# Kernel tuning notes

Hardware: AMD Instinct MI355X
Metric: run time of the kernel (lower is better)

The kernel has to match this reference:

```python
import jax, jax.numpy as jnp
import numpy as np

B, N, K = 4, 2048, 32
H, DS, DE = 128, 128, 128
NUM_IN = DS + DE + H  # 384
SCALE = 30.0
EPS = 1e-5


def setup_inputs() -> dict:
    key = jax.random.key(0)
    ks = jax.random.split(key, 9)
    s = 0.05
    return {
        "h_S": jax.random.normal(ks[0], (B, N, DS), jnp.float32),
        "h_V": jax.random.normal(ks[1], (B, N, H), jnp.float32),
        "h_E": jax.random.normal(ks[2], (B, N, K, DE), jnp.float32),
        "E_idx": jax.random.randint(ks[3], (B, N, K), 0, N, jnp.int64),
        "mask_attend": jnp.ones((B, N, K), jnp.float32),
        "W1_w": jax.random.normal(ks[4], (H + NUM_IN, H), jnp.float32) * s,
        "W1_b": jnp.zeros((H,), jnp.float32),
        "W2_w": jax.random.normal(ks[5], (H, H), jnp.float32) * s,
        "W2_b": jnp.zeros((H,), jnp.float32),
        "ln_g": jnp.ones((H,), jnp.float32),
        "ln_b": jnp.zeros((H,), jnp.float32),
    }


def gather_nodes(nodes, idx):
    # nodes: [B, N, D], idx: [B, N, K] -> [B, N, K, D]
    b, n, k = idx.shape
    d = nodes.shape[-1]
    flat = jnp.broadcast_to(idx.reshape(b, n * k, 1), (b, n * k, d))
    return jnp.take_along_axis(nodes, flat, axis=1).reshape(b, n, k, d)


def layer_norm(x, g, b):
    mu = jnp.mean(x, axis=-1, keepdims=True)
    var = jnp.var(x, axis=-1, keepdims=True)
    return (x - mu) * jax.lax.rsqrt(var + EPS) * g + b


def reference(h_S, h_V, h_E, E_idx, mask_attend, W1_w, W1_b, W2_w, W2_b, ln_g, ln_b):
    # h_ES = cat(h_E, gather(h_S))  -> [B,N,K,DE+DS]
    h_ES = jnp.concatenate([h_E, gather_nodes(h_S, E_idx)], axis=-1)
    # h_EXV = cat(h_ES, gather(h_V)) -> [B,N,K,DE+DS+H], masked
    h_EXV = jnp.concatenate([h_ES, gather_nodes(h_V, E_idx)], axis=-1)
    h_EXV = mask_attend[..., None] * h_EXV
    # h_EV = cat(h_V expanded, h_EXV) -> [B,N,K,H+NUM_IN]
    h_V_exp = jnp.broadcast_to(h_V[:, :, None, :], (h_V.shape[0], h_V.shape[1], K, h_V.shape[2]))
    h_EV = jnp.concatenate([h_V_exp, h_EXV], axis=-1)
    # per-edge 2-layer MLP (exact GELU as torch.nn.GELU)
    h = jax.nn.gelu(jnp.einsum("bnkf,fh->bnkh", h_EV, W1_w) + W1_b, approximate=False)
    h_message = jnp.einsum("bnkh,hg->bnkg", h, W2_w) + W2_b
    dh = jnp.sum(h_message, axis=-2) / SCALE
    # dropout is identity in eval mode
    return layer_norm(h_V + dh, ln_g, ln_b)
```

## Files before the change

### kernel.cpp

```cpp
#include <hip/hip_runtime.h>
#include <math.h>

typedef float f32x4 __attribute__((ext_vector_type(4)));
typedef short s16x8 __attribute__((ext_vector_type(8)));
typedef unsigned u32x4 __attribute__((ext_vector_type(4)));

#define N_NODES 2048
#define KEDGE 32
#define HDIM 128
#define SB() __builtin_amdgcn_sched_barrier(0)

__device__ __forceinline__ short f2bf(float f){
  unsigned u = __builtin_bit_cast(unsigned, f);
  u += 0x7fffu + ((u >> 16) & 1u);
  return (short)(u >> 16);
}
__device__ __forceinline__ float bf2f(short s){
  unsigned u = ((unsigned)(unsigned short)s) << 16;
  return __builtin_bit_cast(float, u);
}
__device__ __forceinline__ unsigned cvt_pk_bf16(float a, float b){
  unsigned r;
  asm("v_cvt_pk_bf16_f32 %0, %1, %2" : "=v"(r) : "v"(a), "v"(b));
  return r;
}
__device__ __forceinline__ float fast_gelu(float x){
  float t = x * (-2.3022078f - 0.1029527f * x * x);
  float e = __builtin_amdgcn_exp2f(t);
  return x * __builtin_amdgcn_rcpf(1.0f + e);
}
__device__ __forceinline__ void gld16(const void* g, void* l){
  __builtin_amdgcn_global_load_lds(
      (const __attribute__((address_space(1))) void*)g,
      (__attribute__((address_space(3))) void*)l, 16, 0, 0);
}
__device__ __forceinline__ f32x4 mfma16(s16x8 a, s16x8 b, f32x4 c){
  return __builtin_amdgcn_mfma_f32_16x16x32_bf16(a, b, c, 0, 0, 0);
}

__global__ void prep1(const float* __restrict__ W1, const float* __restrict__ W2,
                      short* __restrict__ W1f, short* __restrict__ W2f,
                      unsigned* __restrict__ flag){
  if (blockIdx.x == 320){
    if (threadIdx.x == 0) *flag = 0u;
    return;
  }
  int t = blockIdx.x * 256 + threadIdx.x;
  if (t < 65536){
    int ks = t >> 12, r = t & 4095;
    int ct = r >> 9;  r &= 511;
    int lane = r >> 3, j = r & 7;
    int k = ks*32 + (lane>>4)*8 + j;
    int n = ct*16 + (lane&15);
    W1f[t] = f2bf(W1[k*128 + n]);
  } else if (t < 81920){
    int t2 = t - 65536;
    int ks = t2 >> 12, r = t2 & 4095;
    int ct = r >> 9;  r &= 511;
    int lane = r >> 3, j = r & 7;
    int k = ks*32 + (lane>>4)*8 + j;
    int n = ct*16 + (lane&15);
    W2f[t2] = f2bf(W2[k*128 + n]);
  }
}

__global__ __launch_bounds__(256)
void prep2(const float* __restrict__ hS, const float* __restrict__ hV,
           const float* __restrict__ b1, const short* __restrict__ W1f,
           short* __restrict__ Zb, unsigned* __restrict__ UHb,
           const unsigned* __restrict__ Ei_u, unsigned* __restrict__ flag){
  if (blockIdx.x >= 128){
    int t = ((int)blockIdx.x - 128)*256 + threadIdx.x;
    unsigned v = Ei_u[2*t + 1];
    unsigned long long m = __ballot(v != 0u);
    if ((threadIdx.x & 63) == 0 && m) atomicOr(flag, 1u);
    return;
  }
  const int tid = threadIdx.x;
  const int w = tid >> 6, lane = tid & 63, l15 = lane & 15, lg = lane >> 4;
  const int nb = ((int)blockIdx.x*4 + w)*16;

  f32x4 accz[8], accu[8];
  #pragma unroll
  for (int ct = 0; ct < 8; ++ct){ accz[ct] = (f32x4){0,0,0,0}; accu[ct] = (f32x4){0,0,0,0}; }

  #pragma unroll
  for (int ks = 0; ks < 4; ++ks){
    const float* p = hS + (long)(nb + l15)*128 + ks*32 + lg*8;
    float4 x = *(const float4*)p, y = *(const float4*)(p + 4);
    u32x4 pk;
    pk[0] = cvt_pk_bf16(x.x, x.y); pk[1] = cvt_pk_bf16(x.z, x.w);
    pk[2] = cvt_pk_bf16(y.x, y.y); pk[3] = cvt_pk_bf16(y.z, y.w);
    s16x8 a = __builtin_bit_cast(s16x8, pk);
    #pragma unroll
    for (int ct = 0; ct < 8; ++ct){
      s16x8 bf = *(const s16x8*)(W1f + (8+ks)*4096 + ct*512 + lane*8);
      accz[ct] = mfma16(a, bf, accz[ct]);
    }
  }
  #pragma unroll
  for (int ks = 0; ks < 4; ++ks){
    const float* p = hV + (long)(nb + l15)*128 + ks*32 + lg*8;
    float4 x = *(const float4*)p, y = *(const float4*)(p + 4);
    u32x4 pk;
    pk[0] = cvt_pk_bf16(x.x, x.y); pk[1] = cvt_pk_bf16(x.z, x.w);
    pk[2] = cvt_pk_bf16(y.x, y.y); pk[3] = cvt_pk_bf16(y.z, y.w);
    s16x8 a = __builtin_bit_cast(s16x8, pk);
    #pragma unroll
    for (int ct = 0; ct < 8; ++ct){
      s16x8 bfd = *(const s16x8*)(W1f + (12+ks)*4096 + ct*512 + lane*8);
      accz[ct] = mfma16(a, bfd, accz[ct]);
      s16x8 bfa = *(const s16x8*)(W1f + (0+ks)*4096 + ct*512 + lane*8);
      accu[ct] = mfma16(a, bfa, accu[ct]);
    }
  }

  float b1v[8];
  #pragma unroll
  for (int ct = 0; ct < 8; ++ct) b1v[ct] = b1[ct*16 + l15];

  #pragma unroll
  for (int ct = 0; ct < 8; ++ct)
    #pragma unroll
    for (int i = 0; i < 4; ++i){
      const long row = nb + lg*4 + i;
      Zb[row*128 + ct*16 + l15] = f2bf(accz[ct][i]);
      unsigned u16 = (unsigned)(unsigned short)f2bf(accu[ct][i] + b1v[ct]);
      unsigned h16 = (unsigned)(unsigned short)f2bf(hV[row*128 + ct*16 + l15]);
      UHb[row*128 + l15*8 + ct] = u16 | (h16 << 16);
    }
}

__global__ __launch_bounds__(256, 1)
void fusedF(const float* __restrict__ hE, const int* __restrict__ Eidx,
            const float* __restrict__ mask, const short* __restrict__ W1f,
            const short* __restrict__ W2f, const short* __restrict__ Zb,
            const unsigned* __restrict__ UHb, const unsigned* __restrict__ idx_flag,
            const float* __restrict__ W2b, const float* __restrict__ lng,
            const float* __restrict__ lnb, float* __restrict__ out)
{
  __shared__ __align__(16) char smem[69632];

  const int tid  = threadIdx.x;
  const int w    = tid >> 6;
  const int lane = tid & 63;
  const int l15  = lane & 15;
  const int lg   = lane >> 4;

  const int bid  = (int)blockIdx.x;
  const int bswz = (bid & 7)*64 + (bid >> 3);
  const int n0 = (bswz * 4 + w) * 4;
  const long zrow0 = (long)(n0 >> 11) * N_NODES;
  char* mybuf  = smem + w*16384;
  short* vpark = (short*)(smem + 65536 + w*1024);

  const int rr = lane >> 5;
  const unsigned t0 = (unsigned)((rr << 9) | (((lane & 31) << 4) ^ (rr << 4)));

  s16x8 wf[4][8];
  #pragma unroll
  for (int ks = 0; ks < 4; ++ks)
    #pragma unroll
    for (int ct = 0; ct < 8; ++ct)
      wf[ks][ct] = *(const s16x8*)(W1f + (4+ks)*4096 + ct*512 + lane*8);
  SB();

  s16x8 ifr[2];
  #pragma unroll
  for (int c2 = 0; c2 < 2; ++c2){
    const int active = ((lg >> 1) == c2);
    const int j = l15 - 8*(lg & 1);
    s16x8 f;
    #pragma unroll
    for (int e = 0; e < 8; ++e)
      f[e] = (active && j == e) ? (short)0x3F80 : (short)0;
    ifr[c2] = f;
  }

  const int is64 = (*idx_flag == 0u) ? 1 : 0;

  int e0, eZ;
  {
    const int ea = n0*32 + l15;
    const int eb = n0*32 + 16 + l15;
    e0 = Eidx[ea << is64];
    eZ = Eidx[eb << is64];
  }
  float maskC = mask[n0*32 + l15];
  s16x8 uhC[2];
  uhC[0] = *(const s16x8*)((const short*)UHb + (long)n0*256 + l15*16);
  uhC[1] = *(const s16x8*)((const short*)UHb + (long)n0*256 + l15*16 + 8);
  SB();
  #pragma unroll
  for (int q = 0; q < 8; ++q){
    const unsigned off = (unsigned)(q*1024) | (t0 ^ (unsigned)((2*q & 6) << 4));
    gld16((const char*)hE + (size_t)n0*16384 + off, mybuf + q*1024);
  }
  SB();
  s16x8 zbC[4];
  #pragma unroll
  for (int ks = 0; ks < 4; ++ks)
    zbC[ks] = *(const s16x8*)(Zb + (zrow0 + e0)*128 + ks*32 + lg*8);
  SB();
  asm volatile("s_waitcnt vmcnt(0)" ::: "memory");
  SB();

  float vacc[8];
  #pragma unroll
  for (int ct = 0; ct < 8; ++ct) vacc[ct] = 0.f;

  #pragma unroll
  for (int t = 0; t < 8; ++t){
    const int tn = t + 1;
    float maskN = 0.f; s16x8 uhN0{}, uhN1{}; int eN = 0;
    s16x8 zbN0{}, zbN1{}, zbN2{}, zbN3{};
    if (t < 7){
      const int nn_n = n0 + (tn >> 1);
      SB();
      maskN = mask[nn_n*32 + (tn&1)*16 + l15];
      uhN0 = *(const s16x8*)((const short*)UHb + (long)nn_n*256 + l15*16);
      uhN1 = *(const s16x8*)((const short*)UHb + (long)nn_n*256 + l15*16 + 8);
      {
        const int t2 = t + 2;
        const int nz = (t2 <= 7) ? (n0 + (t2>>1)) : n0;
        const int hz = (t2 <= 7) ? (t2&1) : 0;
        eN = Eidx[(nz*32 + hz*16 + l15) << is64];
      }
      SB();
      {
        const size_t eb = (size_t)nn_n*16384 + (size_t)(tn&1)*8192;
        char* sbuf = mybuf + (tn&1)*8192;
        #pragma unroll
        for (int q = 0; q < 8; ++q){
          const unsigned off = (unsigned)(q*1024) | (t0 ^ (unsigned)((2*q & 6) << 4));
          gld16((const char*)hE + eb + off, sbuf + q*1024);
        }
      }
      SB();
      zbN0 = *(const s16x8*)(Zb + (zrow0 + eZ)*128 + 0*32 + lg*8);
      zbN1 = *(const s16x8*)(Zb + (zrow0 + eZ)*128 + 1*32 + lg*8);
      zbN2 = *(const s16x8*)(Zb + (zrow0 + eZ)*128 + 2*32 + lg*8);
      zbN3 = *(const s16x8*)(Zb + (zrow0 + eZ)*128 + 3*32 + lg*8);
      SB();
      asm volatile("s_waitcnt vmcnt(20)" ::: "memory");
      SB();
    } else {
      asm volatile("s_waitcnt vmcnt(0)" ::: "memory");
      SB();
    }

    __builtin_amdgcn_s_setprio(1);

    f32x4 acc1[8];
    #pragma unroll
    for (int ct = 0; ct < 8; ++ct) acc1[ct] = (f32x4){0,0,0,0};

    s16x8 afr[4];
    const char* cbuf = mybuf + (t&1)*8192;
    const int sw = (l15 & 7) << 4;
    const int rowb = l15 * 512;
    #pragma unroll
    for (int ks = 0; ks < 4; ++ks){
      const int c0 = ks*128 + lg*32;
      float4 ex = *(const float4*)(cbuf + rowb + (c0 ^ sw));
      float4 ey = *(const float4*)(cbuf + rowb + ((c0 + 16) ^ sw));
      u32x4 pk;
      pk[0] = cvt_pk_bf16(ex.x, ex.y); pk[1] = cvt_pk_bf16(ex.z, ex.w);
      pk[2] = cvt_pk_bf16(ey.x, ey.y); pk[3] = cvt_pk_bf16(ey.z, ey.w);
      afr[ks] = __builtin_bit_cast(s16x8, pk);
      #pragma unroll
      for (int ct = 0; ct < 8; ++ct)
        acc1[ct] = mfma16(afr[ks], wf[ks][ct], acc1[ct]);
    }

    if (t < 7){
      asm volatile("s_waitcnt vmcnt(16)" ::: "memory");
      SB();
    }

    #pragma unroll
    for (int ks = 0; ks < 4; ++ks)
      #pragma unroll
      for (int c2 = 0; c2 < 2; ++c2)
        acc1[ks*2 + c2] = mfma16(zbC[ks], ifr[c2], acc1[ks*2 + c2]);

    float uv[8];
    #pragma unroll
    for (int ct = 0; ct < 4; ++ct){ uv[ct] = bf2f(uhC[0][2*ct]); uv[4+ct] = bf2f(uhC[1][2*ct]); }
    float mi[4];
    #pragma unroll
    for (int i = 0; i < 4; ++i) mi[i] = __shfl(maskC, lg*4 + i, 64);
    #pragma unroll
    for (int ct = 0; ct < 8; ++ct)
      #pragma unroll
      for (int i = 0; i < 4; ++i)
        vacc[ct] += fast_gelu(uv[ct] + mi[i]*acc1[ct][i]);

    __builtin_amdgcn_s_setprio(0);

    if (t & 1){
      short* vl = vpark + (t >> 1)*128;
      #pragma unroll
      for (int ct = 0; ct < 8; ++ct){
        float s = vacc[ct];
        s += __shfl_xor(s, 16, 64);
        s += __shfl_xor(s, 32, 64);
        vacc[ct] = 0.f;
        if (ct == lg*2 || ct == lg*2 + 1)
          vl[ct*16 + l15] = f2bf(s);
      }
    }

    if (t < 7){
      maskC = maskN; uhC[0] = uhN0; uhC[1] = uhN1; eZ = eN;
      zbC[0] = zbN0; zbC[1] = zbN1; zbC[2] = zbN2; zbC[3] = zbN3;
    }
  }

  asm volatile("s_waitcnt lgkmcnt(0)" ::: "memory");
  SB();

  float w2b8[8], lngv[2], lnbv[2];
  #pragma unroll
  for (int ct = 0; ct < 8; ++ct) w2b8[ct] = W2b[ct*16 + l15];
  #pragma unroll
  for (int q = 0; q < 2; ++q){
    const int c = (lg*2 + q)*16 + l15;
    lngv[q] = lng[c]; lnbv[q] = lnb[c];
  }

  #pragma unroll
  for (int nd = 0; nd < 4; ++nd){
    const short* vl = vpark + nd*128;
    f32x4 acc2[8];
    #pragma unroll
    for (int ct = 0; ct < 8; ++ct) acc2[ct] = (f32x4){0,0,0,0};
    #pragma unroll
    for (int ks2 = 0; ks2 < 4; ++ks2){
      s16x8 av = *(const s16x8*)(vl + ks2*32 + lg*8);
      const short* wb2 = W2f + ks2*4096 + lane*8;
      #pragma unroll
      for (int ct = 0; ct < 8; ++ct){
        s16x8 bf = *(const s16x8*)(wb2 + ct*512);
        acc2[ct] = mfma16(av, bf, acc2[ct]);
      }
    }

    s16x8 uh0 = *(const s16x8*)((const short*)UHb + (long)(n0+nd)*256 + l15*16);
    s16x8 uh1 = *(const s16x8*)((const short*)UHb + (long)(n0+nd)*256 + l15*16 + 8);
    float hv[8];
    #pragma unroll
    for (int ct = 0; ct < 4; ++ct){ hv[ct] = bf2f(uh0[2*ct+1]); hv[4+ct] = bf2f(uh1[2*ct+1]); }

    float res[8], vs = 0.f, vq = 0.f;
    #pragma unroll
    for (int ct = 0; ct < 8; ++ct){
      float dh  = (acc2[ct][0] + 32.0f * w2b8[ct]) * (1.0f/30.0f);
      float val = hv[ct] + dh;
      res[ct] = val;
      vs += val; vq += val*val;
    }
    vs += __shfl_xor(vs, 1, 64);  vs += __shfl_xor(vs, 2, 64);
    vs += __shfl_xor(vs, 4, 64);  vs += __shfl_xor(vs, 8, 64);
    vq += __shfl_xor(vq, 1, 64);  vq += __shfl_xor(vq, 2, 64);
    vq += __shfl_xor(vq, 4, 64);  vq += __shfl_xor(vq, 8, 64);
    const float mu  = vs * (1.0f/128.0f);
    const float var = vq * (1.0f/128.0f) - mu*mu;
    const float rs  = rsqrtf(var + 1e-5f);

    const long nodeoff = (long)(n0 + nd) * HDIM;
    #pragma unroll
    for (int q = 0; q < 2; ++q){
      const int ct = lg*2 + q;
      out[nodeoff + ct*16 + l15] = (res[ct] - mu) * rs * lngv[q] + lnbv[q];
    }
  }
}

extern "C" void kernel_launch(void* const* d_in, const int* in_sizes, int n_in,
                              void* d_out, int out_size, void* d_ws, size_t ws_size,
                              hipStream_t stream) {
  const float* hS  = (const float*)d_in[0];
  const float* hV  = (const float*)d_in[1];
  const float* hE  = (const float*)d_in[2];
  const int*   Ei  = (const int*)d_in[3];
  const float* mk  = (const float*)d_in[4];
  const float* W1w = (const float*)d_in[5];
  const float* W1b = (const float*)d_in[6];
  const float* W2w = (const float*)d_in[7];
  const float* W2b = (const float*)d_in[8];
  const float* lng = (const float*)d_in[9];
  const float* lnb = (const float*)d_in[10];

  short* W1f = (short*)d_ws;
  short* W2f = W1f + 65536;
  unsigned* flag = (unsigned*)((char*)d_ws + 163840);
  short* Zb = (short*)((char*)d_ws + 164096);
  unsigned* UHb = (unsigned*)((char*)d_ws + 2261248);

  prep1<<<321, 256, 0, stream>>>(W1w, W2w, W1f, W2f, flag);
  prep2<<<640, 256, 0, stream>>>(hS, hV, W1b, W1f, Zb, UHb, (const unsigned*)Ei, flag);
  fusedF<<<512, 256, 0, stream>>>(hE, Ei, mk, W1f, W2f, Zb, UHb, flag,
                                  W2b, lng, lnb, (float*)d_out);
}
```

Before: 88.30 us.

## Split each node group across wave pairs, halving per-wave columns and doubling grid

Each group of four nodes is now handled by a pair of waves. Each wave computes half of the output columns, loads half of the hE tile into a shared LDS buffer, and holds half of the W1 fragments in registers. Block barriers synchronize the two halves on the shared LDS buffers, and the grid doubles to 1024 blocks. The aim is lower register and LDS pressure per wave and more parallelism and occupancy, at the cost of extra block-wide barriers and redundant per-team index and mask loads.

```diff
diff --git a/kernel.cpp b/kernel.cpp
--- a/kernel.cpp
+++ b/kernel.cpp
@@ -139,30 +139,33 @@
             const float* __restrict__ W2b, const float* __restrict__ lng,
             const float* __restrict__ lnb, float* __restrict__ out)
 {
-  __shared__ __align__(16) char smem[69632];
+  __shared__ __align__(16) char smem[34816];
 
   const int tid  = threadIdx.x;
   const int w    = tid >> 6;
+  const int team = w >> 1;
+  const int half = w & 1;
+  const int ctb  = half * 4;
   const int lane = tid & 63;
   const int l15  = lane & 15;
   const int lg   = lane >> 4;
 
   const int bid  = (int)blockIdx.x;
-  const int bswz = (bid & 7)*64 + (bid >> 3);
-  const int n0 = (bswz * 4 + w) * 4;
+  const int bswz = (bid & 7)*128 + (bid >> 3);
+  const int n0 = (bswz*2 + team) * 4;
   const long zrow0 = (long)(n0 >> 11) * N_NODES;
-  char* mybuf  = smem + w*16384;
-  short* vpark = (short*)(smem + 65536 + w*1024);
+  char* mybuf  = smem + team*16384;
+  short* vpark = (short*)(smem + 32768 + team*1024);
 
   const int rr = lane >> 5;
   const unsigned t0 = (unsigned)((rr << 9) | (((lane & 31) << 4) ^ (rr << 4)));
 
-  s16x8 wf[4][8];
+  s16x8 wf[4][4];
   #pragma unroll
   for (int ks = 0; ks < 4; ++ks)
     #pragma unroll
-    for (int ct = 0; ct < 8; ++ct)
-      wf[ks][ct] = *(const s16x8*)(W1f + (4+ks)*4096 + ct*512 + lane*8);
+    for (int c = 0; c < 4; ++c)
+      wf[ks][c] = *(const s16x8*)(W1f + (4+ks)*4096 + (ctb+c)*512 + lane*8);
   SB();
 
   s16x8 ifr[2];
@@ -187,39 +190,38 @@
     eZ = Eidx[eb << is64];
   }
   float maskC = mask[n0*32 + l15];
-  s16x8 uhC[2];
-  uhC[0] = *(const s16x8*)((const short*)UHb + (long)n0*256 + l15*16);
-  uhC[1] = *(const s16x8*)((const short*)UHb + (long)n0*256 + l15*16 + 8);
-  SB();
-  #pragma unroll
-  for (int q = 0; q < 8; ++q){
-    const unsigned off = (unsigned)(q*1024) | (t0 ^ (unsigned)((2*q & 6) << 4));
-    gld16((const char*)hE + (size_t)n0*16384 + off, mybuf + q*1024);
-  }
-  SB();
-  s16x8 zbC[4];
-  #pragma unroll
-  for (int ks = 0; ks < 4; ++ks)
-    zbC[ks] = *(const s16x8*)(Zb + (zrow0 + e0)*128 + ks*32 + lg*8);
+  s16x8 uhC = *(const s16x8*)((const short*)UHb + (long)n0*256 + l15*16 + ctb*2);
+  SB();
+  #pragma unroll
+  for (int j = 0; j < 4; ++j){
+    const int qq = half*4 + j;
+    const unsigned off = (unsigned)(qq*1024) | (t0 ^ (unsigned)((2*qq & 6) << 4));
+    gld16((const char*)hE + (size_t)n0*16384 + off, mybuf + qq*1024);
+  }
+  SB();
+  s16x8 zbC[2];
+  #pragma unroll
+  for (int kk = 0; kk < 2; ++kk)
+    zbC[kk] = *(const s16x8*)(Zb + (zrow0 + e0)*128 + (half*2+kk)*32 + lg*8);
   SB();
   asm volatile("s_waitcnt vmcnt(0)" ::: "memory");
   SB();
-
-  float vacc[8];
-  #pragma unroll
-  for (int ct = 0; ct < 8; ++ct) vacc[ct] = 0.f;
+  __builtin_amdgcn_s_barrier();
+
+  float vacc[4];
+  #pragma unroll
+  for (int c = 0; c < 4; ++c) vacc[c] = 0.f;
 
   #pragma unroll
   for (int t = 0; t < 8; ++t){
     const int tn = t + 1;
-    float maskN = 0.f; s16x8 uhN0{}, uhN1{}; int eN = 0;
-    s16x8 zbN0{}, zbN1{}, zbN2{}, zbN3{};
+    float maskN = 0.f; s16x8 uhN{}; int eN = 0;
+    s16x8 zbN0{}, zbN1{};
     if (t < 7){
       const int nn_n = n0 + (tn >> 1);
       SB();
       maskN = mask[nn_n*32 + (tn&1)*16 + l15];
-      uhN0 = *(const s16x8*)((const short*)UHb + (long)nn_n*256 + l15*16);
-      uhN1 = *(const s16x8*)((const short*)UHb + (long)nn_n*256 + l15*16 + 8);
+      uhN = *(const s16x8*)((const short*)UHb + (long)nn_n*256 + l15*16 + ctb*2);
       {
         const int t2 = t + 2;
         const int nz = (t2 <= 7) ? (n0 + (t2>>1)) : n0;
@@ -231,31 +233,30 @@
         const size_t eb = (size_t)nn_n*16384 + (size_t)(tn&1)*8192;
         char* sbuf = mybuf + (tn&1)*8192;
         #pragma unroll
-        for (int q = 0; q < 8; ++q){
-          const unsigned off = (unsigned)(q*1024) | (t0 ^ (unsigned)((2*q & 6) << 4));
-          gld16((const char*)hE + eb + off, sbuf + q*1024);
+        for (int j = 0; j < 4; ++j){
+          const int qq = half*4 + j;
+          const unsigned off = (unsigned)(qq*1024) | (t0 ^ (unsigned)((2*qq & 6) << 4));
+          gld16((const char*)hE + eb + off, sbuf + qq*1024);
         }
       }
       SB();
-      zbN0 = *(const s16x8*)(Zb + (zrow0 + eZ)*128 + 0*32 + lg*8);
-      zbN1 = *(const s16x8*)(Zb + (zrow0 + eZ)*128 + 1*32 + lg*8);
-      zbN2 = *(const s16x8*)(Zb + (zrow0 + eZ)*128 + 2*32 + lg*8);
-      zbN3 = *(const s16x8*)(Zb + (zrow0 + eZ)*128 + 3*32 + lg*8);
-      SB();
-      asm volatile("s_waitcnt vmcnt(20)" ::: "memory");
+      zbN0 = *(const s16x8*)(Zb + (zrow0 + eZ)*128 + (half*2+0)*32 + lg*8);
+      zbN1 = *(const s16x8*)(Zb + (zrow0 + eZ)*128 + (half*2+1)*32 + lg*8);
+      SB();
+      asm volatile("s_waitcnt vmcnt(11)" ::: "memory");
       SB();
     } else {
       asm volatile("s_waitcnt vmcnt(0)" ::: "memory");
       SB();
     }
+    __builtin_amdgcn_s_barrier();
 
     __builtin_amdgcn_s_setprio(1);
 
-    f32x4 acc1[8];
-    #pragma unroll
-    for (int ct = 0; ct < 8; ++ct) acc1[ct] = (f32x4){0,0,0,0};
-
-    s16x8 afr[4];
+    f32x4 acc1[4];
+    #pragma unroll
+    for (int c = 0; c < 4; ++c) acc1[c] = (f32x4){0,0,0,0};
+
     const char* cbuf = mybuf + (t&1)*8192;
     const int sw = (l15 & 7) << 4;
     const int rowb = l15 * 512;
@@ -267,58 +268,59 @@
       u32x4 pk;
       pk[0] = cvt_pk_bf16(ex.x, ex.y); pk[1] = cvt_pk_bf16(ex.z, ex.w);
       pk[2] = cvt_pk_bf16(ey.x, ey.y); pk[3] = cvt_pk_bf16(ey.z, ey.w);
-      afr[ks] = __builtin_bit_cast(s16x8, pk);
+      s16x8 a = __builtin_bit_cast(s16x8, pk);
       #pragma unroll
-      for (int ct = 0; ct < 8; ++ct)
-        acc1[ct] = mfma16(afr[ks], wf[ks][ct], acc1[ct]);
+      for (int c = 0; c < 4; ++c)
+        acc1[c] = mfma16(a, wf[ks][c], acc1[c]);
     }
 
     if (t < 7){
-      asm volatile("s_waitcnt vmcnt(16)" ::: "memory");
-      SB();
-    }
-
-    #pragma unroll
-    for (int ks = 0; ks < 4; ++ks)
+      asm volatile("s_waitcnt vmcnt(9)" ::: "memory");
+      SB();
+    }
+
+    #pragma unroll
+    for (int kk = 0; kk < 2; ++kk)
       #pragma unroll
       for (int c2 = 0; c2 < 2; ++c2)
-        acc1[ks*2 + c2] = mfma16(zbC[ks], ifr[c2], acc1[ks*2 + c2]);
-
-    float uv[8];
-    #pragma unroll
-    for (int ct = 0; ct < 4; ++ct){ uv[ct] = bf2f(uhC[0][2*ct]); uv[4+ct] = bf2f(uhC[1][2*ct]); }
+        acc1[kk*2 + c2] = mfma16(zbC[kk], ifr[c2], acc1[kk*2 + c2]);
+
+    float uv[4];
+    #pragma unroll
+    for (int c = 0; c < 4; ++c) uv[c] = bf2f(uhC[2*c]);
     float mi[4];
     #pragma unroll
     for (int i = 0; i < 4; ++i) mi[i] = __shfl(maskC, lg*4 + i, 64);
     #pragma unroll
-    for (int ct = 0; ct < 8; ++ct)
+    for (int c = 0; c < 4; ++c)
       #pragma unroll
       for (int i = 0; i < 4; ++i)
-        vacc[ct] += fast_gelu(uv[ct] + mi[i]*acc1[ct][i]);
+        vacc[c] += fast_gelu(uv[c] + mi[i]*acc1[c][i]);
 
     __builtin_amdgcn_s_setprio(0);
 
     if (t & 1){
       short* vl = vpark + (t >> 1)*128;
       #pragma unroll
-      for (int ct = 0; ct < 8; ++ct){
-        float s = vacc[ct];
+      for (int c = 0; c < 4; ++c){
+        float s = vacc[c];
         s += __shfl_xor(s, 16, 64);
         s += __shfl_xor(s, 32, 64);
-        vacc[ct] = 0.f;
-        if (ct == lg*2 || ct == lg*2 + 1)
-          vl[ct*16 + l15] = f2bf(s);
+        vacc[c] = 0.f;
+        if (lg == c)
+          vl[(ctb + c)*16 + l15] = f2bf(s);
       }
     }
 
     if (t < 7){
-      maskC = maskN; uhC[0] = uhN0; uhC[1] = uhN1; eZ = eN;
-      zbC[0] = zbN0; zbC[1] = zbN1; zbC[2] = zbN2; zbC[3] = zbN3;
+      maskC = maskN; uhC = uhN; eZ = eN;
+      zbC[0] = zbN0; zbC[1] = zbN1;
     }
   }
 
   asm volatile("s_waitcnt lgkmcnt(0)" ::: "memory");
   SB();
+  __builtin_amdgcn_s_barrier();
 
   float w2b8[8], lngv[2], lnbv[2];
   #pragma unroll
@@ -330,7 +332,8 @@
   }
 
   #pragma unroll
-  for (int nd = 0; nd < 4; ++nd){
+  for (int j = 0; j < 2; ++j){
+    const int nd = half*2 + j;
     const short* vl = vpark + nd*128;
     f32x4 acc2[8];
     #pragma unroll
@@ -350,7 +353,7 @@
     s16x8 uh1 = *(const s16x8*)((const short*)UHb + (long)(n0+nd)*256 + l15*16 + 8);
     float hv[8];
     #pragma unroll
-    for (int ct = 0; ct < 4; ++ct){ hv[ct] = bf2f(uh0[2*ct+1]); hv[4+ct] = bf2f(uh1[2*ct+1]); }
+    for (int c = 0; c < 4; ++c){ hv[c] = bf2f(uh0[2*c+1]); hv[4+c] = bf2f(uh1[2*c+1]); }
 
     float res[8], vs = 0.f, vq = 0.f;
     #pragma unroll
@@ -400,6 +403,6 @@
 
   prep1<<<321, 256, 0, stream>>>(W1w, W2w, W1f, W2f, flag);
   prep2<<<640, 256, 0, stream>>>(hS, hV, W1b, W1f, Zb, UHb, (const unsigned*)Ei, flag);
-  fusedF<<<512, 256, 0, stream>>>(hE, Ei, mk, W1f, W2f, Zb, UHb, flag,
-                                  W2b, lng, lnb, (float*)d_out);
-}
+  fusedF<<<1024, 256, 0, stream>>>(hE, Ei, mk, W1f, W2f, Zb, UHb, flag,
+                                   W2b, lng, lnb, (float*)d_out);
+}
```

After: 81.36 us. 1.09x faster.
